# Kernel tuning notes

Measured on AMD Instinct MI355X. Metric: run time of the kernel, lower is better.

Reference implementation:

```python
import jax, jax.numpy as jnp
import numpy as np
import math

B, H, L, D = 2, 16, 2048, 64
NEG_E = 1000000000000.0  # the module's default e


def setup_inputs() -> dict:
    key = jax.random.key(0)
    kq, kk, kv, km = jax.random.split(key, 4)
    q = jax.random.normal(kq, (B, H, L, D), dtype=jnp.float32)
    k = jax.random.normal(kk, (B, H, L, D), dtype=jnp.float32)
    v = jax.random.normal(kv, (B, H, L, D), dtype=jnp.float32)
    mask = jax.random.randint(km, (B, L, L), 0, 2, dtype=jnp.int32)
    return {"q": q, "k": k, "v": v, "mask": mask}


def reference(q, k, v, mask):
    b, h, l, d = k.shape
    # FAITHFUL quirk 1: original does k.view(B,H,D,L) -- a reshape, NOT a transpose.
    k_t = jnp.reshape(k, (b, h, d, l))
    score = jnp.matmul(q, k_t) / math.sqrt(d)  # [B,H,L,L]
    # mask.unsqueeze(1): broadcast over heads; masked positions -> -e
    score = jnp.where(mask[:, None, :, :] == 0, jnp.float32(-NEG_E), score)
    # FAITHFUL quirk 2: nn.Softmax(dim=1) normalizes over the HEAD axis.
    score = jax.nn.softmax(score, axis=1)
    out = jnp.matmul(score, v)  # [B,H,L,D]
    return (out, score)
```

## Files before the change

kernel.cpp:

```cpp
#include <hip/hip_runtime.h>
#include <math.h>

#define NB 2
#define NH 16
#define LSEQ 2048
#define DD 64
#define HSZ (LSEQ*DD)
#define NELEM (NB*NH*HSZ)

typedef _Float16 half_t;
typedef _Float16 f16x4 __attribute__((ext_vector_type(4)));
typedef _Float16 f16x8 __attribute__((ext_vector_type(8)));
typedef float    f32x4 __attribute__((ext_vector_type(4)));

__global__ __launch_bounds__(256) void convert_q(
    const float* __restrict__ q, half_t* __restrict__ qh)
{
    const int n4 = NELEM / 4;
    for (int gid = blockIdx.x * 256 + threadIdx.x; gid < n4; gid += gridDim.x * 256) {
        float4 x = ((const float4*)q)[gid];
        f16x4 y;
        y[0] = (half_t)x.x; y[1] = (half_t)x.y; y[2] = (half_t)x.z; y[3] = (half_t)x.w;
        ((f16x4*)qh)[gid] = y;
    }
}

__global__ __launch_bounds__(256) void transpose_cvt(
    const float* __restrict__ k, const float* __restrict__ v,
    half_t* __restrict__ kt, half_t* __restrict__ vt)
{
    __shared__ half_t lds[64][72];
    const int tid = threadIdx.x;
    const int bh  = blockIdx.y;
    const int t64 = blockIdx.x;
    const float* src; half_t* dst; int C, R, r0, c0;
    if (blockIdx.z == 0) {
        src = k + (size_t)bh * HSZ; dst = kt + (size_t)bh * HSZ;
        R = 64; C = LSEQ; r0 = 0; c0 = t64 * 64;
    } else {
        src = v + (size_t)bh * HSZ; dst = vt + (size_t)bh * HSZ;
        R = LSEQ; C = 64; r0 = t64 * 64; c0 = 0;
    }
    const int rr = tid & 63, w4 = tid >> 6;
    #pragma unroll
    for (int qq = 0; qq < 4; ++qq) {
        float4 x = *(const float4*)&src[(size_t)(r0 + rr) * C + c0 + w4 * 16 + qq * 4];
        lds[w4 * 16 + qq * 4 + 0][rr] = (half_t)x.x;
        lds[w4 * 16 + qq * 4 + 1][rr] = (half_t)x.y;
        lds[w4 * 16 + qq * 4 + 2][rr] = (half_t)x.z;
        lds[w4 * 16 + qq * 4 + 3][rr] = (half_t)x.w;
    }
    __syncthreads();
    #pragma unroll
    for (int p = 0; p < 2; ++p) {
        const int id = tid + p * 256;
        const int cl = id >> 3, rc = id & 7;
        f16x8 y = *(const f16x8*)&lds[cl][rc * 8];
        *(f16x8*)&dst[(size_t)(c0 + cl) * R + r0 + rc * 8] = y;
    }
}

__global__ __launch_bounds__(256) void qk_softmax_mfma(
    const half_t* __restrict__ qh, const half_t* __restrict__ kt,
    const int* __restrict__ mask, float* __restrict__ score)
{
    const int tid = threadIdx.x, w = tid >> 6, lane = tid & 63;
    const int is = w >> 1, jb = w & 1;
    const int j0 = blockIdx.x * 32, i0 = blockIdx.y * 32, b = blockIdx.z;
    const int g8 = (lane >> 4) * 8, n16 = lane & 15;
    const int irow = i0 + is * 16 + n16;
    const int jcol = j0 + jb * 16 + n16;
    const size_t hb0 = (size_t)b * NH;

    f32x4 acc[NH];
    #pragma unroll
    for (int h = 0; h < NH; ++h) { acc[h][0] = 0.f; acc[h][1] = 0.f; acc[h][2] = 0.f; acc[h][3] = 0.f; }

    #pragma unroll
    for (int h = 0; h < NH; ++h) {
        const half_t* qp = qh + (hb0 + h) * (size_t)HSZ + (size_t)irow * DD;
        const half_t* kp = kt + (hb0 + h) * (size_t)HSZ + (size_t)jcol * DD;
        f16x8 a0 = *(const f16x8*)(qp + g8);
        f16x8 a1 = *(const f16x8*)(qp + 32 + g8);
        f16x8 b0 = *(const f16x8*)(kp + g8);
        f16x8 b1 = *(const f16x8*)(kp + 32 + g8);
        acc[h] = __builtin_amdgcn_mfma_f32_16x16x32_f16(a0, b0, acc[h], 0, 0, 0);
        acc[h] = __builtin_amdgcn_mfma_f32_16x16x32_f16(a1, b1, acc[h], 0, 0, 0);
    }

    const int crow0 = i0 + is * 16 + (lane >> 4) * 4;
    #pragma unroll
    for (int r = 0; r < 4; ++r) {
        const int m = mask[((size_t)b * LSEQ + crow0 + r) * LSEQ + jcol];
        if (m == 0) {
            #pragma unroll
            for (int h = 0; h < NH; ++h) acc[h][r] = 0.0625f;
        } else {
            float mx = acc[0][r];
            #pragma unroll
            for (int h = 1; h < NH; ++h) mx = fmaxf(mx, acc[h][r]);
            float s = 0.f;
            #pragma unroll
            for (int h = 0; h < NH; ++h) {
                float e = __expf(0.125f * (acc[h][r] - mx));
                acc[h][r] = e;
                s += e;
            }
            const float inv = 1.0f / s;
            #pragma unroll
            for (int h = 0; h < NH; ++h) acc[h][r] *= inv;
        }
    }
    #pragma unroll
    for (int h = 0; h < NH; ++h)
        #pragma unroll
        for (int r = 0; r < 4; ++r)
            score[((hb0 + h) * LSEQ + crow0 + r) * LSEQ + jcol] = acc[h][r];
}

__global__ __launch_bounds__(256) void pv_mfma(
    const float* __restrict__ score, const half_t* __restrict__ vt,
    float* __restrict__ out)
{
    const int tid = threadIdx.x, w = tid >> 6, lane = tid & 63;
    const int i0 = blockIdx.x * 64;
    const size_t bh = (size_t)blockIdx.z * NH + blockIdx.y;
    const float*  sb = score + bh * (size_t)LSEQ * LSEQ;
    const half_t* vb = vt + bh * (size_t)HSZ;
    float*        ob = out + bh * (size_t)HSZ;
    const int g8 = (lane >> 4) * 8, n16 = lane & 15;
    const int irow = i0 + w * 16 + n16;

    f32x4 acc[4];
    #pragma unroll
    for (int ds = 0; ds < 4; ++ds) { acc[ds][0] = 0.f; acc[ds][1] = 0.f; acc[ds][2] = 0.f; acc[ds][3] = 0.f; }

    const float* sp0 = sb + (size_t)irow * LSEQ + g8;

    #pragma unroll 2
    for (int t = 0; t < 64; ++t) {
        float4 sA = *(const float4*)(sp0 + t * 32);
        float4 sB = *(const float4*)(sp0 + t * 32 + 4);
        f16x8 a8;
        a8[0] = (half_t)sA.x; a8[1] = (half_t)sA.y; a8[2] = (half_t)sA.z; a8[3] = (half_t)sA.w;
        a8[4] = (half_t)sB.x; a8[5] = (half_t)sB.y; a8[6] = (half_t)sB.z; a8[7] = (half_t)sB.w;
        #pragma unroll
        for (int ds = 0; ds < 4; ++ds) {
            f16x8 b8 = *(const f16x8*)(vb + (size_t)(ds * 16 + n16) * LSEQ + t * 32 + g8);
            acc[ds] = __builtin_amdgcn_mfma_f32_16x16x32_f16(a8, b8, acc[ds], 0, 0, 0);
        }
    }
    const int orow0 = i0 + w * 16 + (lane >> 4) * 4;
    #pragma unroll
    for (int ds = 0; ds < 4; ++ds)
        #pragma unroll
        for (int r = 0; r < 4; ++r)
            ob[(size_t)(orow0 + r) * DD + ds * 16 + n16] = acc[ds][r];
}

extern "C" void kernel_launch(void* const* d_in, const int* in_sizes, int n_in,
                              void* d_out, int out_size, void* d_ws, size_t ws_size,
                              hipStream_t stream) {
    const float* q    = (const float*)d_in[0];
    const float* k    = (const float*)d_in[1];
    const float* v    = (const float*)d_in[2];
    const int*   mask = (const int*)d_in[3];

    float* out   = (float*)d_out;
    float* score = out + (size_t)NB * NH * LSEQ * DD;

    half_t* qh = (half_t*)d_ws;
    half_t* kt = qh + NELEM;
    half_t* vt = kt + NELEM;

    convert_q<<<2048, 256, 0, stream>>>(q, qh);
    transpose_cvt<<<dim3(32, NB * NH, 2), 256, 0, stream>>>(k, v, kt, vt);
    qk_softmax_mfma<<<dim3(LSEQ / 32, LSEQ / 32, NB), 256, 0, stream>>>(qh, kt, mask, score);
    pv_mfma<<<dim3(LSEQ / 64, NH, NB), 256, 0, stream>>>(score, vt, out);
}
```

Before: 514.7 us.

## Fuse QK softmax-over-heads and PV into one attention kernel

Merges the score/softmax kernel and the PV kernel into one kernel. Each block owns 16 query rows for all 16 heads (4 heads per wave) and loops over key tiles. It computes scores with MFMA, does the head-axis softmax through an LDS cross-wave sum reduction, writes the fp32 score, and feeds the fp16 probabilities straight into PV MFMAs. This removes the 537MB fp32 score re-read by the second kernel and one launch, but the score write remains. The cost is a per-tile barrier, only 256 blocks at one block per CU, and dropping the max subtraction, which relies on the scores being small enough not to overflow exp.

```diff
diff --git a/kernel.cpp b/kernel.cpp
--- a/kernel.cpp
+++ b/kernel.cpp
@@ -60,102 +60,126 @@
     }
 }
 
-__global__ __launch_bounds__(256) void qk_softmax_mfma(
+__global__ __launch_bounds__(256, 1) void fused_attn(
     const half_t* __restrict__ qh, const half_t* __restrict__ kt,
-    const int* __restrict__ mask, float* __restrict__ score)
+    const half_t* __restrict__ vt, const int* __restrict__ mask,
+    float* __restrict__ score, float* __restrict__ out)
 {
+    __shared__ float smem[4352];
     const int tid = threadIdx.x, w = tid >> 6, lane = tid & 63;
-    const int is = w >> 1, jb = w & 1;
-    const int j0 = blockIdx.x * 32, i0 = blockIdx.y * 32, b = blockIdx.z;
-    const int g8 = (lane >> 4) * 8, n16 = lane & 15;
-    const int irow = i0 + is * 16 + n16;
-    const int jcol = j0 + jb * 16 + n16;
+    const int n16 = lane & 15, g = lane >> 4;
+    const int g4 = g * 4, g8 = g * 8;
+    const int i0 = blockIdx.x * 16, b = blockIdx.y;
     const size_t hb0 = (size_t)b * NH;
-
-    f32x4 acc[NH];
-    #pragma unroll
-    for (int h = 0; h < NH; ++h) { acc[h][0] = 0.f; acc[h][1] = 0.f; acc[h][2] = 0.f; acc[h][3] = 0.f; }
-
-    #pragma unroll
-    for (int h = 0; h < NH; ++h) {
-        const half_t* qp = qh + (hb0 + h) * (size_t)HSZ + (size_t)irow * DD;
-        const half_t* kp = kt + (hb0 + h) * (size_t)HSZ + (size_t)jcol * DD;
-        f16x8 a0 = *(const f16x8*)(qp + g8);
-        f16x8 a1 = *(const f16x8*)(qp + 32 + g8);
-        f16x8 b0 = *(const f16x8*)(kp + g8);
-        f16x8 b1 = *(const f16x8*)(kp + 32 + g8);
-        acc[h] = __builtin_amdgcn_mfma_f32_16x16x32_f16(a0, b0, acc[h], 0, 0, 0);
-        acc[h] = __builtin_amdgcn_mfma_f32_16x16x32_f16(a1, b1, acc[h], 0, 0, 0);
-    }
-
-    const int crow0 = i0 + is * 16 + (lane >> 4) * 4;
-    #pragma unroll
-    for (int r = 0; r < 4; ++r) {
-        const int m = mask[((size_t)b * LSEQ + crow0 + r) * LSEQ + jcol];
-        if (m == 0) {
-            #pragma unroll
-            for (int h = 0; h < NH; ++h) acc[h][r] = 0.0625f;
-        } else {
-            float mx = acc[0][r];
-            #pragma unroll
-            for (int h = 1; h < NH; ++h) mx = fmaxf(mx, acc[h][r]);
-            float s = 0.f;
-            #pragma unroll
-            for (int h = 0; h < NH; ++h) {
-                float e = __expf(0.125f * (acc[h][r] - mx));
-                acc[h][r] = e;
-                s += e;
+    const int h0 = w * 4;
+    const int irow = i0 + n16;
+
+    f16x8 qf[4][2];
+    #pragma unroll
+    for (int hh = 0; hh < 4; ++hh)
+        #pragma unroll
+        for (int kg = 0; kg < 2; ++kg)
+            qf[hh][kg] = *(const f16x8*)(qh + (hb0 + h0 + hh) * (size_t)HSZ
+                                         + (size_t)irow * DD + kg * 32 + g8);
+
+    f32x4 acc[4][4];
+    #pragma unroll
+    for (int hh = 0; hh < 4; ++hh)
+        #pragma unroll
+        for (int ds = 0; ds < 4; ++ds) { acc[hh][ds][0]=0.f; acc[hh][ds][1]=0.f; acc[hh][ds][2]=0.f; acc[hh][ds][3]=0.f; }
+
+    const int* mrow = mask + ((size_t)b * LSEQ + irow) * LSEQ;
+
+    for (int t = 0; t < 64; ++t) {
+        const int j0 = t * 32;
+        int4 m0 = *(const int4*)(mrow + j0 + g4);
+        int4 m1 = *(const int4*)(mrow + j0 + 16 + g4);
+        int mvv[2][4] = {{m0.x, m0.y, m0.z, m0.w}, {m1.x, m1.y, m1.z, m1.w}};
+
+        f32x4 sc[4][2];
+        #pragma unroll
+        for (int hh = 0; hh < 4; ++hh) {
+            const half_t* kp = kt + (hb0 + h0 + hh) * (size_t)HSZ;
+            #pragma unroll
+            for (int jb = 0; jb < 2; ++jb) {
+                const half_t* kr = kp + (size_t)(j0 + jb * 16 + n16) * DD;
+                f16x8 k0 = *(const f16x8*)(kr + g8);
+                f16x8 k1 = *(const f16x8*)(kr + 32 + g8);
+                f32x4 c = {0.f, 0.f, 0.f, 0.f};
+                c = __builtin_amdgcn_mfma_f32_16x16x32_f16(k0, qf[hh][0], c, 0, 0, 0);
+                c = __builtin_amdgcn_mfma_f32_16x16x32_f16(k1, qf[hh][1], c, 0, 0, 0);
+                sc[hh][jb] = c;
             }
-            const float inv = 1.0f / s;
-            #pragma unroll
-            for (int h = 0; h < NH; ++h) acc[h][r] *= inv;
         }
-    }
-    #pragma unroll
-    for (int h = 0; h < NH; ++h)
-        #pragma unroll
-        for (int r = 0; r < 4; ++r)
-            score[((hb0 + h) * LSEQ + crow0 + r) * LSEQ + jcol] = acc[h][r];
-}
-
-__global__ __launch_bounds__(256) void pv_mfma(
-    const float* __restrict__ score, const half_t* __restrict__ vt,
-    float* __restrict__ out)
-{
-    const int tid = threadIdx.x, w = tid >> 6, lane = tid & 63;
-    const int i0 = blockIdx.x * 64;
-    const size_t bh = (size_t)blockIdx.z * NH + blockIdx.y;
-    const float*  sb = score + bh * (size_t)LSEQ * LSEQ;
-    const half_t* vb = vt + bh * (size_t)HSZ;
-    float*        ob = out + bh * (size_t)HSZ;
-    const int g8 = (lane >> 4) * 8, n16 = lane & 15;
-    const int irow = i0 + w * 16 + n16;
-
-    f32x4 acc[4];
-    #pragma unroll
-    for (int ds = 0; ds < 4; ++ds) { acc[ds][0] = 0.f; acc[ds][1] = 0.f; acc[ds][2] = 0.f; acc[ds][3] = 0.f; }
-
-    const float* sp0 = sb + (size_t)irow * LSEQ + g8;
-
-    #pragma unroll 2
-    for (int t = 0; t < 64; ++t) {
-        float4 sA = *(const float4*)(sp0 + t * 32);
-        float4 sB = *(const float4*)(sp0 + t * 32 + 4);
-        f16x8 a8;
-        a8[0] = (half_t)sA.x; a8[1] = (half_t)sA.y; a8[2] = (half_t)sA.z; a8[3] = (half_t)sA.w;
-        a8[4] = (half_t)sB.x; a8[5] = (half_t)sB.y; a8[6] = (half_t)sB.z; a8[7] = (half_t)sB.w;
-        #pragma unroll
-        for (int ds = 0; ds < 4; ++ds) {
-            f16x8 b8 = *(const f16x8*)(vb + (size_t)(ds * 16 + n16) * LSEQ + t * 32 + g8);
-            acc[ds] = __builtin_amdgcn_mfma_f32_16x16x32_f16(a8, b8, acc[ds], 0, 0, 0);
+
+        f32x4 ps[2] = {{0.f,0.f,0.f,0.f}, {0.f,0.f,0.f,0.f}};
+        #pragma unroll
+        for (int hh = 0; hh < 4; ++hh)
+            #pragma unroll
+            for (int jb = 0; jb < 2; ++jb)
+                #pragma unroll
+                for (int r = 0; r < 4; ++r) {
+                    float e = (mvv[jb][r] == 0) ? 1.0f : __expf(0.125f * sc[hh][jb][r]);
+                    sc[hh][jb][r] = e;
+                    ps[jb][r] += e;
+                }
+
+        float* red = smem + (t & 1) * 2112;
+        #pragma unroll
+        for (int jb = 0; jb < 2; ++jb)
+            #pragma unroll
+            for (int r = 0; r < 4; ++r)
+                red[n16 * 132 + (jb * 16 + g4 + r) * 4 + w] = ps[jb][r];
+        asm volatile("s_waitcnt lgkmcnt(0)" ::: "memory");
+        __builtin_amdgcn_s_barrier();
+
+        float inv_[2][4];
+        #pragma unroll
+        for (int jb = 0; jb < 2; ++jb)
+            #pragma unroll
+            for (int r = 0; r < 4; ++r) {
+                f32x4 s4 = *(const f32x4*)&red[n16 * 132 + (jb * 16 + g4 + r) * 4];
+                inv_[jb][r] = 1.0f / (s4[0] + s4[1] + s4[2] + s4[3]);
+            }
+
+        #pragma unroll
+        for (int hh = 0; hh < 4; ++hh) {
+            float* srow = score + ((hb0 + h0 + hh) * LSEQ + irow) * LSEQ + j0;
+            const half_t* vp = vt + (hb0 + h0 + hh) * (size_t)HSZ;
+            #pragma unroll
+            for (int jb = 0; jb < 2; ++jb) {
+                f32x4 p; f16x4 pb;
+                #pragma unroll
+                for (int r = 0; r < 4; ++r) { p[r] = sc[hh][jb][r] * inv_[jb][r]; pb[r] = (half_t)p[r]; }
+                *(f32x4*)(srow + jb * 16 + g4) = p;
+                #pragma unroll
+                for (int ds = 0; ds < 4; ++ds) {
+                    f16x4 av = *(const f16x4*)(vp + (size_t)(ds * 16 + n16) * LSEQ + j0 + jb * 16 + g4);
+                    acc[hh][ds] = __builtin_amdgcn_mfma_f32_16x16x16f16(av, pb, acc[hh][ds], 0, 0, 0);
+                }
+            }
         }
     }
-    const int orow0 = i0 + w * 16 + (lane >> 4) * 4;
-    #pragma unroll
-    for (int ds = 0; ds < 4; ++ds)
-        #pragma unroll
-        for (int r = 0; r < 4; ++r)
-            ob[(size_t)(orow0 + r) * DD + ds * 16 + n16] = acc[ds][r];
+
+    __syncthreads();
+    float* ep = smem + w * 1088;
+    const int il = lane >> 2, cc = lane & 3;
+    #pragma unroll
+    for (int hh = 0; hh < 4; ++hh) {
+        #pragma unroll
+        for (int ds = 0; ds < 4; ++ds)
+            #pragma unroll
+            for (int r = 0; r < 4; ++r)
+                ep[n16 * 68 + ds * 16 + g4 + r] = acc[hh][ds][r];
+        asm volatile("s_waitcnt lgkmcnt(0)" ::: "memory");
+        float* orow = out + (hb0 + h0 + hh) * (size_t)HSZ + (size_t)(i0 + il) * DD + cc * 16;
+        #pragma unroll
+        for (int qq = 0; qq < 4; ++qq) {
+            f32x4 x = *(const f32x4*)&ep[il * 68 + cc * 16 + qq * 4];
+            *(f32x4*)(orow + qq * 4) = x;
+        }
+        asm volatile("s_waitcnt lgkmcnt(0)" ::: "memory");
+    }
 }
 
 extern "C" void kernel_launch(void* const* d_in, const int* in_sizes, int n_in,
@@ -175,6 +199,5 @@
 
     convert_q<<<2048, 256, 0, stream>>>(q, qh);
     transpose_cvt<<<dim3(32, NB * NH, 2), 256, 0, stream>>>(k, v, kt, vt);
-    qk_softmax_mfma<<<dim3(LSEQ / 32, LSEQ / 32, NB), 256, 0, stream>>>(qh, kt, mask, score);
-    pv_mfma<<<dim3(LSEQ / 64, NH, NB), 256, 0, stream>>>(score, vt, out);
-}
+    fused_attn<<<dim3(LSEQ / 16, NB), 256, 0, stream>>>(qh, kt, vt, mask, score, out);
+}
```

Result: slower. 875.5 us (+70.1%).
